# Optimization experiments

Hardware: AMD Instinct MI355X
Metric: run time of the kernel (lower is better)

Reference implementation:

```python
import jax, jax.numpy as jnp
import numpy as np

B, S, DIM, COV = 64, 512, 1024, 256


def setup_inputs() -> dict:
    key = jax.random.key(0)
    ks = jax.random.split(key, 12)
    s = 0.02
    h = jax.random.normal(ks[0], (B, DIM), jnp.float32)
    context = jax.random.normal(ks[1], (B, S, DIM), jnp.float32)
    cov = jax.random.normal(ks[2], (B, S, COV), jnp.float32)
    mask = jax.random.randint(ks[3], (B, S), 0, 2) == 1
    W_in = jax.random.normal(ks[4], (DIM, DIM), jnp.float32) * s
    W_out = jax.random.normal(ks[5], (DIM, 2 * DIM), jnp.float32) * s
    W_cov = jax.random.normal(ks[6], (DIM, COV), jnp.float32) * s
    b_cov = jax.random.normal(ks[7], (DIM,), jnp.float32) * s
    w_ih = jax.random.normal(ks[8], (3 * COV, 2 * DIM + 1), jnp.float32) * s
    w_hh = jax.random.normal(ks[9], (3 * COV, COV), jnp.float32) * s
    b_ih = jax.random.normal(ks[10], (3 * COV,), jnp.float32) * s
    b_hh = jax.random.normal(ks[11], (3 * COV,), jnp.float32) * s
    return dict(h=h, context=context, cov=cov, W_in=W_in, W_out=W_out,
                W_cov=W_cov, b_cov=b_cov, w_ih=w_ih, w_hh=w_hh,
                b_ih=b_ih, b_hh=b_hh, mask=mask)


def reference(h, context, cov, W_in, W_out, W_cov, b_cov, w_ih, w_hh, b_ih, b_hh, mask):
    # coverage-adjusted context: context + cov_linear(cov)  [B,S,DIM]
    ctx = context + jnp.einsum('bsc,dc->bsd', cov, W_cov) + b_cov
    # target = linear_in(h)  [B,DIM]
    target = h @ W_in.T
    # scores = bmm(context, target).squeeze(2)  [B,S]
    attn = jnp.einsum('bsd,bd->bs', ctx, target)
    attn = jnp.where(mask, -jnp.inf, attn)
    attn = jax.nn.softmax(attn, axis=1)
    # weighted_context = bmm(attn3, context)  [B,DIM]
    wc = jnp.einsum('bs,bsd->bd', attn, ctx)
    h_tilde = jnp.tanh(jnp.concatenate([wc, h], axis=1) @ W_out.T)
    # single-step GRU coverage update over B*S rows
    h_exp = jnp.broadcast_to(h[:, None, :], (B, S, DIM))
    x = jnp.concatenate([ctx, h_exp, attn[..., None]], axis=-1).reshape(B * S, 2 * DIM + 1)
    h0 = cov.reshape(B * S, COV)
    gx = x @ w_ih.T + b_ih   # [B*S, 3*COV]
    gh = h0 @ w_hh.T + b_hh  # [B*S, 3*COV]
    xr, xz, xn = jnp.split(gx, 3, axis=1)
    hr, hz, hn = jnp.split(gh, 3, axis=1)
    r = jax.nn.sigmoid(xr + hr)
    z = jax.nn.sigmoid(xz + hz)
    n = jnp.tanh(xn + r * hn)
    new_cov = ((1.0 - z) * n + z * h0).reshape(B, S, COV)
    return h_tilde, attn, new_cov
```

## Files before the change

### kernel.cpp

```cpp
#include <hip/hip_runtime.h>
#include <math.h>

typedef unsigned short ushort_t;
typedef __attribute__((ext_vector_type(8))) short short8;
typedef __attribute__((ext_vector_type(4))) float f32x4;
typedef __attribute__((ext_vector_type(4))) unsigned short ushort4v;

constexpr int B_ = 64, S_ = 512, DIM_ = 1024, COV_ = 256, TC_ = 768, KIH_ = 2049;
constexpr int NG_ = 1024, KG_ = 1280;

__device__ __forceinline__ float b2f(ushort_t u) {
    union { unsigned int i; float f; } v; v.i = ((unsigned int)u) << 16; return v.f;
}
__device__ __forceinline__ ushort_t f2b(float f) {
    unsigned int x = __float_as_uint(f);
    unsigned int r = x + 0x7fffu + ((x >> 16) & 1u);
    return (ushort_t)(r >> 16);
}
__device__ __forceinline__ float ldv(const float* p, size_t i) { return p[i]; }
__device__ __forceinline__ float ldv(const ushort_t* p, size_t i) { return b2f(p[i]); }

__device__ __forceinline__ float wave_reduce(float a) {
#pragma unroll
    for (int off = 32; off >= 1; off >>= 1) a += __shfl_down(a, off, 64);
    return a;
}

__device__ __forceinline__ void xpose4(f32x4& v, int l) {
    float s, r;
    s = (l & 1) ? v[0] : v[1]; r = __shfl_xor(s, 1, 64); if (l & 1) v[0] = r; else v[1] = r;
    s = (l & 1) ? v[2] : v[3]; r = __shfl_xor(s, 1, 64); if (l & 1) v[2] = r; else v[3] = r;
    s = (l & 2) ? v[0] : v[2]; r = __shfl_xor(s, 2, 64); if (l & 2) v[0] = r; else v[2] = r;
    s = (l & 2) ? v[1] : v[3]; r = __shfl_xor(s, 2, 64); if (l & 2) v[1] = r; else v[3] = r;
}

#define GLDS16(src, dst)                                                            \
    __builtin_amdgcn_global_load_lds(                                               \
        (const __attribute__((address_space(1))) void*)(src),                       \
        (__attribute__((address_space(3))) void*)(dst), 16, 0, 0)

__global__ void k_detect(const unsigned char* __restrict__ mask,
                         const ushort_t* __restrict__ win,
                         int* __restrict__ flags) {
    __shared__ int red0[256];
    __shared__ int red1[256];
    int tid = threadIdx.x, mb = 0, f32 = 0;
    for (int i = tid; i < 32768; i += 256)
        if ((i & 3) != 0 && mask[i] != 0) mb = 1;
    for (int i = tid; i < 32768; i += 256) {
        ushort_t u = win[2 * i];
        if ((u & 0x7F80u) >= 0x4480u) f32 = 1;
    }
    red0[tid] = mb; red1[tid] = f32; __syncthreads();
    for (int st = 128; st >= 1; st >>= 1) {
        if (tid < st) { red0[tid] |= red0[tid + st]; red1[tid] |= red1[tid + st]; }
        __syncthreads();
    }
    if (tid == 0) { flags[0] = red0[0]; flags[1] = red1[0]; }
}

template <typename IT>
__device__ __forceinline__ void transpose_body(const IT* __restrict__ in,
                                               ushort_t* __restrict__ out,
                                               int R, int C, int ld, int off) {
    int idx = blockIdx.x * 256 + threadIdx.x;
    if (idx >= R * C) return;
    int r = idx / C, c = idx - r * C;
    out[c * R + r] = f2b(ldv(in, (size_t)r * ld + off + c));
}
__global__ void k_transpose(const void* __restrict__ in, ushort_t* __restrict__ out,
                            int R, int C, int ld, int off, const int* __restrict__ flags) {
    if (flags[1]) transpose_body((const float*)in, out, R, C, ld, off);
    else transpose_body((const ushort_t*)in, out, R, C, ld, off);
}

template <typename IT>
__device__ __forceinline__ void watt_body(const IT* __restrict__ wih, float* __restrict__ watt) {
    int j = threadIdx.x;
    watt[j] = ldv(wih, (size_t)j * KIH_ + 2048);
}
__global__ void k_watt(const void* __restrict__ wih, float* __restrict__ watt,
                       const int* __restrict__ flags) {
    if (flags[1]) watt_body((const float*)wih, watt);
    else watt_body((const ushort_t*)wih, watt);
}

template <typename IT>
__device__ __forceinline__ void bfold_body(const IT* __restrict__ bcov,
                                           const IT* __restrict__ wih,
                                           float* __restrict__ bfold) {
    int j = blockIdx.x * 4 + (threadIdx.x >> 6);
    int lane = threadIdx.x & 63;
    const IT* wr = wih + (size_t)j * KIH_;
    float a = 0.f;
#pragma unroll
    for (int i = 0; i < 16; ++i) { int k = lane + 64 * i; a += ldv(bcov, k) * ldv(wr, k); }
    a = wave_reduce(a);
    if (lane == 0) bfold[j] = a;
}
__global__ __launch_bounds__(256) void k_bfold(const void* __restrict__ bcov,
                                               const void* __restrict__ wih,
                                               float* __restrict__ bfold,
                                               const int* __restrict__ flags) {
    if (flags[1]) bfold_body((const float*)bcov, (const float*)wih, bfold);
    else bfold_body((const ushort_t*)bcov, (const ushort_t*)wih, bfold);
}

__global__ __launch_bounds__(256) void k_wfold(const ushort_t* __restrict__ wcov_t,
                                               const ushort_t* __restrict__ w_t,
                                               float* __restrict__ wfold) {
    __shared__ float col[DIM_];
    int c = blockIdx.x, tid = threadIdx.x;
    for (int d = tid; d < DIM_; d += 256) col[d] = b2f(wcov_t[c * DIM_ + d]);
    __syncthreads();
    float a0 = 0.f, a1 = 0.f, a2 = 0.f;
    for (int d = 0; d < DIM_; ++d) {
        float x = col[d];
        const ushort_t* wr = w_t + d * TC_;
        a0 += x * b2f(wr[tid]);
        a1 += x * b2f(wr[tid + 256]);
        a2 += x * b2f(wr[tid + 512]);
    }
    wfold[c * TC_ + tid] = a0;
    wfold[c * TC_ + tid + 256] = a1;
    wfold[c * TC_ + tid + 512] = a2;
}

template <typename IT>
__device__ __forceinline__ void buildwg_body(const IT* __restrict__ wih,
                                             const IT* __restrict__ whh,
                                             const float* __restrict__ wfold,
                                             ushort_t* __restrict__ wg) {
    int idx = blockIdx.x * 256 + threadIdx.x;
    if (idx >= NG_ * KG_) return;
    int n = idx / KG_, k = idx - n * KG_;
    int g = n & 3, cq = n >> 2;
    int j = g * COV_ + cq;
    float v;
    if (k < DIM_) {
        v = (j < TC_) ? ldv(wih, (size_t)j * KIH_ + k) : 0.f;
    } else {
        int c = k - DIM_;
        if (j < 512)      v = wfold[c * TC_ + j] + ldv(whh, (size_t)j * COV_ + c);
        else if (j < TC_) v = wfold[c * TC_ + j];
        else              v = ldv(whh, (size_t)(j - 256) * COV_ + c);
    }
    wg[(size_t)n * KG_ + k] = f2b(v);
}
__global__ void k_buildwg(const void* __restrict__ wih, const void* __restrict__ whh,
                          const float* __restrict__ wfold, ushort_t* __restrict__ wg,
                          const int* __restrict__ flags) {
    if (flags[1]) buildwg_body((const float*)wih, (const float*)whh, wfold, wg);
    else buildwg_body((const ushort_t*)wih, (const ushort_t*)whh, wfold, wg);
}

template <typename IT>
__device__ __forceinline__ void target_body(const IT* __restrict__ h,
                                            const IT* __restrict__ W_in,
                                            float* __restrict__ target) {
    int o = blockIdx.x * 4 + (threadIdx.x >> 6);
    int lane = threadIdx.x & 63;
    int b = o >> 10, d = o & (DIM_ - 1);
    const IT* hr = h + (size_t)b * DIM_;
    const IT* wr = W_in + (size_t)d * DIM_;
    float a = 0.f;
#pragma unroll
    for (int j = 0; j < 16; ++j) { int k = lane + 64 * j; a += ldv(hr, k) * ldv(wr, k); }
    a = wave_reduce(a);
    if (lane == 0) target[o] = a;
}
__global__ __launch_bounds__(256) void k_target_w(const void* __restrict__ h,
                                                  const void* __restrict__ W_in,
                                                  float* __restrict__ target,
                                                  const int* __restrict__ flags) {
    if (flags[1]) target_body((const float*)h, (const float*)W_in, target);
    else target_body((const ushort_t*)h, (const ushort_t*)W_in, target);
}

template <typename IT>
__device__ __forceinline__ void mvec_body(const float* __restrict__ target,
                                          const IT* __restrict__ W_cov,
                                          const IT* __restrict__ bcov,
                                          float* __restrict__ mvec,
                                          float* __restrict__ bct) {
    __shared__ float tg[DIM_];
    __shared__ float red[256];
    int b = blockIdx.x, q = blockIdx.y, tid = threadIdx.x;
    float pb = 0.f;
    for (int k = tid; k < DIM_; k += 256) {
        float t = target[b * DIM_ + k];
        tg[k] = t; pb += t * ldv(bcov, k);
    }
    red[tid] = pb; __syncthreads();
    for (int st = 128; st >= 1; st >>= 1) {
        if (tid < st) red[tid] += red[tid + st];
        __syncthreads();
    }
    if (q == 0 && tid == 0) bct[b] = red[0];
    __syncthreads();
    int cg = tid & 63, dg = tid >> 6;
    int c = q * 64 + cg;
    float acc = 0.f;
    int d0 = dg * 256;
    for (int d = d0; d < d0 + 256; ++d) acc += tg[d] * ldv(W_cov, (size_t)d * COV_ + c);
    red[dg * 64 + cg] = acc;
    __syncthreads();
    if (dg == 0)
        mvec[b * COV_ + c] = red[cg] + red[64 + cg] + red[128 + cg] + red[192 + cg];
}
__global__ __launch_bounds__(256) void k_mvec(const float* __restrict__ target,
                                              const void* __restrict__ W_cov,
                                              const void* __restrict__ bcov,
                                              float* __restrict__ mvec,
                                              float* __restrict__ bct,
                                              const int* __restrict__ flags) {
    if (flags[1]) mvec_body(target, (const float*)W_cov, (const float*)bcov, mvec, bct);
    else mvec_body(target, (const ushort_t*)W_cov, (const ushort_t*)bcov, mvec, bct);
}

template <typename IT>
__device__ __forceinline__ void scoreraw_body(const IT* __restrict__ context,
                                              const IT* __restrict__ cov,
                                              const float* __restrict__ target,
                                              const float* __restrict__ mvec,
                                              const float* __restrict__ bct,
                                              float* __restrict__ scf,
                                              ushort_t* __restrict__ ctx_bf,
                                              ushort_t* __restrict__ cov_bf) {
    __shared__ float tg[DIM_];
    __shared__ float ms[COV_];
    int b = blockIdx.x, tid = threadIdx.x;
    for (int k = tid; k < DIM_; k += 256) tg[k] = target[b * DIM_ + k];
    if (tid < COV_) ms[tid] = mvec[b * COV_ + tid];
    float bc = bct[b];
    __syncthreads();
    int wave = tid >> 6, lane = tid & 63;
    int s0 = blockIdx.y * 64 + wave * 16;
    for (int i = 0; i < 16; ++i) {
        int s = s0 + i;
        size_t row = (size_t)(b * S_ + s);
        const IT* cr = context + row * DIM_;
        const IT* vr = cov + row * COV_;
        float a = 0.f;
        if constexpr (sizeof(IT) == 4) {
#pragma unroll
            for (int j = 0; j < 4; ++j) {
                int d = lane * 4 + 256 * j;
                float4 x = *(const float4*)((const float*)cr + d);
                a += x.x * tg[d] + x.y * tg[d + 1] + x.z * tg[d + 2] + x.w * tg[d + 3];
                if (ctx_bf) {
                    ushort4v u;
                    u[0] = f2b(x.x); u[1] = f2b(x.y); u[2] = f2b(x.z); u[3] = f2b(x.w);
                    *(ushort4v*)(ctx_bf + row * DIM_ + d) = u;
                }
            }
            {
                int cc = lane * 4;
                float4 x = *(const float4*)((const float*)vr + cc);
                a += x.x * ms[cc] + x.y * ms[cc + 1] + x.z * ms[cc + 2] + x.w * ms[cc + 3];
                if (cov_bf) {
                    ushort4v u;
                    u[0] = f2b(x.x); u[1] = f2b(x.y); u[2] = f2b(x.z); u[3] = f2b(x.w);
                    *(ushort4v*)(cov_bf + row * COV_ + cc) = u;
                }
            }
        } else {
#pragma unroll
            for (int j = 0; j < 16; ++j) { int d = lane + 64 * j; a += ldv(cr, d) * tg[d]; }
#pragma unroll
            for (int j = 0; j < 4; ++j) { int c = lane + 64 * j; a += ldv(vr, c) * ms[c]; }
        }
        a = wave_reduce(a);
        if (lane == 0) scf[row] = a + bc;
    }
}
__global__ __launch_bounds__(256) void k_scoreraw(const void* __restrict__ context,
                                                  const void* __restrict__ cov,
                                                  const float* __restrict__ target,
                                                  const float* __restrict__ mvec,
                                                  const float* __restrict__ bct,
                                                  float* __restrict__ scf,
                                                  ushort_t* __restrict__ ctx_bf,
                                                  ushort_t* __restrict__ cov_bf,
                                                  const int* __restrict__ flags) {
    if (flags[1]) scoreraw_body((const float*)context, (const float*)cov, target, mvec, bct,
                                scf, ctx_bf, cov_bf);
    else scoreraw_body((const ushort_t*)context, (const ushort_t*)cov, target, mvec, bct,
                       scf, ctx_bf, cov_bf);
}

__global__ __launch_bounds__(256) void k_softmax(const float* __restrict__ scf,
                                                 const void* __restrict__ maskp,
                                                 const int* __restrict__ flags,
                                                 float* __restrict__ attnf,
                                                 float* __restrict__ attn_out) {
    __shared__ float red[256];
    int b = blockIdx.x, tid = threadIdx.x;
    int mb = flags[0];
    int i0 = b * S_ + tid, i1 = i0 + 256;
    int m0 = mb ? (int)((const unsigned char*)maskp)[i0] : ((const int*)maskp)[i0];
    int m1 = mb ? (int)((const unsigned char*)maskp)[i1] : ((const int*)maskp)[i1];
    float s0 = m0 ? -INFINITY : scf[i0];
    float s1 = m1 ? -INFINITY : scf[i1];
    red[tid] = fmaxf(s0, s1); __syncthreads();
    for (int st = 128; st >= 1; st >>= 1) {
        if (tid < st) red[tid] = fmaxf(red[tid], red[tid + st]);
        __syncthreads();
    }
    float mx = red[0]; __syncthreads();
    float e0 = expf(s0 - mx), e1 = expf(s1 - mx);
    red[tid] = e0 + e1; __syncthreads();
    for (int st = 128; st >= 1; st >>= 1) {
        if (tid < st) red[tid] += red[tid + st];
        __syncthreads();
    }
    float inv = 1.0f / red[0];
    float a0 = e0 * inv, a1 = e1 * inv;
    attnf[i0] = a0; attnf[i1] = a1;
    attn_out[i0] = a0; attn_out[i1] = a1;
}

__global__ __launch_bounds__(256) void k_wcpart2(const ushort_t* __restrict__ ctx_bf,
                                                 const ushort_t* __restrict__ cov_bf,
                                                 const void* __restrict__ ctx_in,
                                                 const void* __restrict__ cov_in,
                                                 const float* __restrict__ attnf,
                                                 float* __restrict__ wc8,
                                                 float* __restrict__ ac8,
                                                 const int* __restrict__ flags) {
    const ushort_t* C = flags[1] ? ctx_bf : (const ushort_t*)ctx_in;
    const ushort_t* V = flags[1] ? cov_bf : (const ushort_t*)cov_in;
    __shared__ float at[64];
    int b = blockIdx.x, ch = blockIdx.y, tid = threadIdx.x;
    int s0 = ch * 64;
    if (tid < 64) at[tid] = attnf[b * S_ + s0 + tid];
    __syncthreads();
    float acv = 0.f;
    for (int s = 0; s < 64; ++s)
        acv += at[s] * b2f(V[((size_t)(b * S_ + s0 + s)) * COV_ + tid]);
    ac8[((size_t)ch * B_ + b) * COV_ + tid] = acv;
    float acc[4] = {0.f, 0.f, 0.f, 0.f};
    for (int s = 0; s < 64; ++s) {
        float w = at[s];
        const ushort_t* cr = C + ((size_t)(b * S_ + s0 + s)) * DIM_;
        acc[0] += w * b2f(cr[tid]);
        acc[1] += w * b2f(cr[tid + 256]);
        acc[2] += w * b2f(cr[tid + 512]);
        acc[3] += w * b2f(cr[tid + 768]);
    }
    size_t base = ((size_t)ch * B_ + b) * DIM_;
    for (int m = 0; m < 4; ++m) wc8[base + tid + 256 * m] = acc[m];
}

template <typename IT>
__device__ __forceinline__ void wcfin_body(const float* __restrict__ wc8,
                                           const float* __restrict__ ac8,
                                           const ushort_t* __restrict__ wcov_t,
                                           const IT* __restrict__ bcov,
                                           float* __restrict__ wc) {
    __shared__ float ac[COV_];
    int b = blockIdx.x, tid = threadIdx.x;
    float a = 0.f;
    for (int ch = 0; ch < 8; ++ch) a += ac8[((size_t)ch * B_ + b) * COV_ + tid];
    ac[tid] = a;
    __syncthreads();
    float acc[4] = {0.f, 0.f, 0.f, 0.f};
    for (int ch = 0; ch < 8; ++ch) {
        size_t base = ((size_t)ch * B_ + b) * DIM_;
        for (int m = 0; m < 4; ++m) acc[m] += wc8[base + tid + 256 * m];
    }
    for (int c = 0; c < COV_; ++c) {
        float av = ac[c];
        const ushort_t* wr = wcov_t + c * DIM_;
        acc[0] += av * b2f(wr[tid]);
        acc[1] += av * b2f(wr[tid + 256]);
        acc[2] += av * b2f(wr[tid + 512]);
        acc[3] += av * b2f(wr[tid + 768]);
    }
    for (int m = 0; m < 4; ++m) {
        int d = tid + 256 * m;
        wc[b * DIM_ + d] = acc[m] + ldv(bcov, d);
    }
}
__global__ __launch_bounds__(256) void k_wcfin(const float* __restrict__ wc8,
                                               const float* __restrict__ ac8,
                                               const ushort_t* __restrict__ wcov_t,
                                               const void* __restrict__ bcov,
                                               float* __restrict__ wc,
                                               const int* __restrict__ flags) {
    if (flags[1]) wcfin_body(wc8, ac8, wcov_t, (const float*)bcov, wc);
    else wcfin_body(wc8, ac8, wcov_t, (const ushort_t*)bcov, wc);
}

template <typename IT>
__device__ __forceinline__ void htilde_body(const float* __restrict__ wc,
                                            const IT* __restrict__ h,
                                            const IT* __restrict__ W_out,
                                            float* __restrict__ out_ht) {
    int o = blockIdx.x * 4 + (threadIdx.x >> 6);
    int lane = threadIdx.x & 63;
    int b = o >> 10, d = o & (DIM_ - 1);
    const float* wcr = wc + b * DIM_;
    const IT* hr = h + (size_t)b * DIM_;
    const IT* wr = W_out + (size_t)d * 2 * DIM_;
    float a = 0.f;
#pragma unroll
    for (int j = 0; j < 16; ++j) { int k = lane + 64 * j; a += wcr[k] * ldv(wr, k); }
#pragma unroll
    for (int j = 0; j < 16; ++j) { int k = lane + 64 * j; a += ldv(hr, k) * ldv(wr, DIM_ + k); }
    a = wave_reduce(a);
    if (lane == 0) out_ht[o] = tanhf(a);
}
__global__ __launch_bounds__(256) void k_htilde_w(const float* __restrict__ wc,
                                                  const void* __restrict__ h,
                                                  const void* __restrict__ W_out,
                                                  float* __restrict__ out_ht,
                                                  const int* __restrict__ flags) {
    if (flags[1]) htilde_body(wc, (const float*)h, (const float*)W_out, out_ht);
    else htilde_body(wc, (const ushort_t*)h, (const ushort_t*)W_out, out_ht);
}

template <typename IT>
__device__ __forceinline__ void gxh_body(const IT* __restrict__ h,
                                         const IT* __restrict__ w_ih,
                                         const IT* __restrict__ b_ih,
                                         const float* __restrict__ bfold,
                                         float* __restrict__ gxall) {
    int o = blockIdx.x * 4 + (threadIdx.x >> 6);
    int lane = threadIdx.x & 63;
    int b = o / TC_, j = o - b * TC_;
    const IT* hr = h + (size_t)b * DIM_;
    const IT* wr = w_ih + (size_t)j * KIH_ + DIM_;
    float a = 0.f;
#pragma unroll
    for (int i = 0; i < 16; ++i) { int k = lane + 64 * i; a += ldv(hr, k) * ldv(wr, k); }
    a = wave_reduce(a);
    if (lane == 0) gxall[o] = a + ldv(b_ih, j) + bfold[j];
}
__global__ __launch_bounds__(256) void k_gxh_w(const void* __restrict__ h,
                                               const void* __restrict__ w_ih,
                                               const void* __restrict__ b_ih,
                                               const float* __restrict__ bfold,
                                               float* __restrict__ gxall,
                                               const int* __restrict__ flags) {
    if (flags[1]) gxh_body((const float*)h, (const float*)w_ih, (const float*)b_ih, bfold, gxall);
    else gxh_body((const ushort_t*)h, (const ushort_t*)w_ih, (const ushort_t*)b_ih, bfold, gxall);
}

__global__ __launch_bounds__(256) void k_gemm6(const ushort_t* __restrict__ ctx_bf,
                                               const ushort_t* __restrict__ cov_bf,
                                               const void* __restrict__ ctx_in,
                                               const void* __restrict__ cov_in,
                                               const ushort_t* __restrict__ wg,
                                               const float* __restrict__ attnf,
                                               const float* __restrict__ gxall,
                                               const float* __restrict__ watt,
                                               const void* __restrict__ bhh,
                                               float* __restrict__ out_cov,
                                               const int* __restrict__ flags) {
    const int f32in = flags[1];
    const ushort_t* Xc = f32in ? ctx_bf : (const ushort_t*)ctx_in;
    const ushort_t* Xv = f32in ? cov_bf : (const ushort_t*)cov_in;
    __shared__ __align__(16) unsigned char smem[65536];
    ushort_t* A0 = (ushort_t*)smem;
    ushort_t* B0 = A0 + 8192;
    ushort_t* A1 = B0 + 8192;
    ushort_t* B1 = A1 + 8192;
    float* smN = (float*)smem;
    float* smZ = smN + 128 * 33;

    int tid = threadIdx.x;
    int p = blockIdx.x;
    int xcd = p & 7, t = p >> 3;
    int nb = t & 7, rb = xcd + 8 * (t >> 3);
    int n0 = nb * 128;
    int grow0 = rb * 128;
    int wave = tid >> 6, lane = tid & 63;
    int wm = wave >> 1, wn = wave & 1;
    int half = lane >> 4, r16 = lane & 15;

    const ushort_t* gAc[4]; const ushort_t* gAv[4]; const ushort_t* gB[4];
    int ldsOff[4];
#pragma unroll
    for (int j = 0; j < 4; ++j) {
        int c = wave * 256 + j * 64 + lane;
        int row = c >> 3, sl = (c & 7) ^ ((c >> 3) & 7);
        gAc[j] = Xc + (size_t)(grow0 + row) * DIM_ + sl * 8;
        gAv[j] = Xv + (size_t)(grow0 + row) * COV_ + sl * 8;
        gB[j]  = wg + (size_t)(n0 + row) * KG_ + sl * 8;
        ldsOff[j] = (wave * 256 + j * 64) * 8;
    }

    int offA[2][4], offB[2][4];
#pragma unroll
    for (int kh = 0; kh < 2; ++kh)
#pragma unroll
        for (int u = 0; u < 4; ++u) {
            int rA = wm * 64 + u * 16 + r16;
            offA[kh][u] = rA * 64 + ((kh * 4 + half) ^ (rA & 7)) * 8;
            int rB = wn * 64 + u * 16 + r16;
            offB[kh][u] = rB * 64 + ((kh * 4 + half) ^ (rB & 7)) * 8;
        }

    f32x4 acc[4][4];
#pragma unroll
    for (int i = 0; i < 4; ++i)
#pragma unroll
        for (int j = 0; j < 4; ++j) acc[i][j] = (f32x4){0.f, 0.f, 0.f, 0.f};

    auto stage = [&](int kt, ushort_t* Ad, ushort_t* Bd) {
        int k0 = kt * 64;
        if (k0 < DIM_) {
#pragma unroll
            for (int j = 0; j < 4; ++j) GLDS16(gAc[j] + k0, Ad + ldsOff[j]);
        } else {
            int kk = k0 - DIM_;
#pragma unroll
            for (int j = 0; j < 4; ++j) GLDS16(gAv[j] + kk, Ad + ldsOff[j]);
        }
#pragma unroll
        for (int j = 0; j < 4; ++j) GLDS16(gB[j] + k0, Bd + ldsOff[j]);
    };
    auto compute = [&](const ushort_t* Ac, const ushort_t* Bc) {
#pragma unroll
        for (int kh = 0; kh < 2; ++kh) {
            short8 a[4], b[4];
#pragma unroll
            for (int u = 0; u < 4; ++u) a[u] = *(const short8*)&Ac[offA[kh][u]];
#pragma unroll
            for (int u = 0; u < 4; ++u) b[u] = *(const short8*)&Bc[offB[kh][u]];
#pragma unroll
            for (int i = 0; i < 4; ++i)
#pragma unroll
                for (int j = 0; j < 4; ++j)
                    acc[i][j] = __builtin_amdgcn_mfma_f32_16x16x32_bf16(a[i], b[j], acc[i][j], 0, 0, 0);
        }
    };

    constexpr int NT = KG_ / 64;
    stage(0, A0, B0);
    __syncthreads();
#pragma unroll 1
    for (int kt = 0; kt < NT; kt += 2) {
        stage(kt + 1, A1, B1);
        compute(A0, B0);
        __syncthreads();
        if (kt + 2 < NT) stage(kt + 2, A0, B0);
        compute(A1, B1);
        __syncthreads();
    }

    int l = lane;
    int bb = grow0 >> 9;
    const float* gx = gxall + bb * TC_;
    int rloc[4]; float atv[4];
#pragma unroll
    for (int i = 0; i < 4; ++i) {
        rloc[i] = wm * 64 + 16 * i + ((l >> 4) << 2) + (l & 3);
        atv[i] = attnf[grow0 + rloc[i]];
    }
#pragma unroll
    for (int j = 0; j < 4; ++j) {
        int cl = wn * 16 + 4 * j + ((l >> 2) & 3);
        int c = (n0 >> 2) + cl;
        float gxR = gx[c], gxZ = gx[COV_ + c], gxN = gx[2 * COV_ + c];
        float waR = watt[c], waZ = watt[COV_ + c], waN = watt[2 * COV_ + c];
        float bhR, bhZ, bhN;
        if (f32in) {
            const float* bp = (const float*)bhh;
            bhR = bp[c]; bhZ = bp[COV_ + c]; bhN = bp[2 * COV_ + c];
        } else {
            const ushort_t* bp = (const ushort_t*)bhh;
            bhR = b2f(bp[c]); bhZ = b2f(bp[COV_ + c]); bhN = b2f(bp[2 * COV_ + c]);
        }
#pragma unroll
        for (int i = 0; i < 4; ++i) {
            f32x4 v = acc[i][j];
            xpose4(v, l);
            float at = atv[i];
            float aR  = v[0] + gxR + at * waR + bhR;
            float aZ  = v[1] + gxZ + at * waZ + bhZ;
            float aXN = v[2] + gxN + at * waN;
            float aHN = v[3] + bhN;
            float r = 1.f / (1.f + expf(-aR));
            float z = 1.f / (1.f + expf(-aZ));
            float nn = tanhf(aXN + r * aHN);
            smN[rloc[i] * 33 + cl] = nn;
            smZ[rloc[i] * 33 + cl] = z;
        }
    }
    __syncthreads();
    int cbase = nb * 32;
    for (int u = tid; u < 128 * 8; u += 256) {
        int rl = u >> 3, c4 = (u & 7) * 4;
        float n0v = smN[rl * 33 + c4 + 0], n1v = smN[rl * 33 + c4 + 1];
        float n2v = smN[rl * 33 + c4 + 2], n3v = smN[rl * 33 + c4 + 3];
        float z0 = smZ[rl * 33 + c4 + 0], z1 = smZ[rl * 33 + c4 + 1];
        float z2 = smZ[rl * 33 + c4 + 2], z3 = smZ[rl * 33 + c4 + 3];
        size_t base = (size_t)(grow0 + rl) * COV_ + cbase + c4;
        float h0v, h1v, h2v, h3v;
        if (f32in) {
            float4 hv = *(const float4*)((const float*)cov_in + base);
            h0v = hv.x; h1v = hv.y; h2v = hv.z; h3v = hv.w;
        } else {
            ushort4v hv = *(const ushort4v*)((const ushort_t*)cov_in + base);
            h0v = b2f(hv[0]); h1v = b2f(hv[1]); h2v = b2f(hv[2]); h3v = b2f(hv[3]);
        }
        float4 o;
        o.x = (1.f - z0) * n0v + z0 * h0v;
        o.y = (1.f - z1) * n1v + z1 * h1v;
        o.z = (1.f - z2) * n2v + z2 * h2v;
        o.w = (1.f - z3) * n3v + z3 * h3v;
        *(float4*)(out_cov + base) = o;
    }
}

template <typename IT>
__device__ __forceinline__ void gru_body(const IT* __restrict__ context,
                                         const IT* __restrict__ cov,
                                         const float* __restrict__ attnf,
                                         const float* __restrict__ gxall,
                                         const float* __restrict__ watt,
                                         const ushort_t* __restrict__ w_t,
                                         const float* __restrict__ wfold,
                                         const ushort_t* __restrict__ whh_t,
                                         const IT* __restrict__ bhh,
                                         float* __restrict__ out_cov) {
    __shared__ float xc[8][DIM_];
    __shared__ float h0s[8][COV_];
    __shared__ float atn[8];
    int base = blockIdx.x * 8, tid = threadIdx.x;
    int b = base / S_;
    for (int i = tid; i < 8 * DIM_; i += 256)
        ((float*)xc)[i] = ldv(context, (size_t)base * DIM_ + i);
    for (int i = tid; i < 8 * COV_; i += 256)
        ((float*)h0s)[i] = ldv(cov, (size_t)base * COV_ + i);
    if (tid < 8) atn[tid] = attnf[base + tid];
    __syncthreads();
    int c = tid;
    float gxR = gxall[b * TC_ + c], gxZ = gxall[b * TC_ + 256 + c], gxN = gxall[b * TC_ + 512 + c];
    float bhR = ldv(bhh, c), bhZ = ldv(bhh, 256 + c), bhN = ldv(bhh, 512 + c);
    float waR = watt[c], waZ = watt[256 + c], waN = watt[512 + c];
    float aR[8], aZ[8], aXN[8], aHN[8];
#pragma unroll
    for (int g = 0; g < 8; ++g) {
        float a = atn[g];
        aR[g] = gxR + bhR + a * waR;
        aZ[g] = gxZ + bhZ + a * waZ;
        aXN[g] = gxN + a * waN;
        aHN[g] = bhN;
    }
    for (int k = 0; k < DIM_; ++k) {
        const ushort_t* row = w_t + k * TC_;
        float wr = b2f(row[c]), wz = b2f(row[256 + c]), wn = b2f(row[512 + c]);
#pragma unroll
        for (int g = 0; g < 8; ++g) {
            float x = xc[g][k];
            aR[g] += x * wr; aZ[g] += x * wz; aXN[g] += x * wn;
        }
    }
    for (int k = 0; k < COV_; ++k) {
        const float* row = wfold + k * TC_;
        float wr = row[c], wz = row[256 + c], wn = row[512 + c];
#pragma unroll
        for (int g = 0; g < 8; ++g) {
            float x = h0s[g][k];
            aR[g] += x * wr; aZ[g] += x * wz; aXN[g] += x * wn;
        }
    }
    for (int k = 0; k < COV_; ++k) {
        const ushort_t* row = whh_t + k * TC_;
        float wr = b2f(row[c]), wz = b2f(row[256 + c]), wn = b2f(row[512 + c]);
#pragma unroll
        for (int g = 0; g < 8; ++g) {
            float hh = h0s[g][k];
            aR[g] += hh * wr; aZ[g] += hh * wz; aHN[g] += hh * wn;
        }
    }
#pragma unroll
    for (int g = 0; g < 8; ++g) {
        float r = 1.f / (1.f + expf(-aR[g]));
        float z = 1.f / (1.f + expf(-aZ[g]));
        float n = tanhf(aXN[g] + r * aHN[g]);
        float h0c = h0s[g][c];
        out_cov[(size_t)(base + g) * COV_ + c] = (1.f - z) * n + z * h0c;
    }
}
__global__ __launch_bounds__(256) void k_gru_f(const void* __restrict__ context,
                                               const void* __restrict__ cov,
                                               const float* __restrict__ attnf,
                                               const float* __restrict__ gxall,
                                               const float* __restrict__ watt,
                                               const ushort_t* __restrict__ w_t,
                                               const float* __restrict__ wfold,
                                               const ushort_t* __restrict__ whh_t,
                                               const void* __restrict__ bhh,
                                               float* __restrict__ out_cov,
                                               const int* __restrict__ flags) {
    if (flags[1]) gru_body((const float*)context, (const float*)cov, attnf, gxall, watt,
                           w_t, wfold, whh_t, (const float*)bhh, out_cov);
    else gru_body((const ushort_t*)context, (const ushort_t*)cov, attnf, gxall, watt,
                  w_t, wfold, whh_t, (const ushort_t*)bhh, out_cov);
}

extern "C" void kernel_launch(void* const* d_in, const int* in_sizes, int n_in,
                              void* d_out, int out_size, void* d_ws, size_t ws_size,
                              hipStream_t stream) {
    const void* h       = d_in[0];
    const void* context = d_in[1];
    const void* cov     = d_in[2];
    const void* W_in    = d_in[3];
    const void* W_out   = d_in[4];
    const void* W_cov   = d_in[5];
    const void* b_cov   = d_in[6];
    const void* w_ih    = d_in[7];
    const void* w_hh    = d_in[8];
    const void* b_ih    = d_in[9];
    const void* b_hh    = d_in[10];
    const void* maskp   = d_in[11];

    float* out = (float*)d_out;
    float* out_ht   = out;
    float* out_attn = out + B_ * DIM_;
    float* out_cov  = out + B_ * DIM_ + B_ * S_;

    char* ws = (char*)d_ws;
    size_t o = 0;
    float* target = (float*)(ws + o); o += (size_t)B_ * DIM_ * 4;
    float* attnf  = (float*)(ws + o); o += (size_t)B_ * S_ * 4;
    float* wc     = (float*)(ws + o); o += (size_t)B_ * DIM_ * 4;
    float* gxall  = (float*)(ws + o); o += (size_t)B_ * TC_ * 4;
    float* watt   = (float*)(ws + o); o += 4096;
    float* mvec   = (float*)(ws + o); o += (size_t)B_ * COV_ * 4;
    float* bct    = (float*)(ws + o); o += 4096;
    float* bfold  = (float*)(ws + o); o += 4096;
    float* wfold  = (float*)(ws + o); o += (size_t)COV_ * TC_ * 4;
    ushort_t* w_t    = (ushort_t*)(ws + o); o += (size_t)DIM_ * TC_ * 2;
    ushort_t* whh_t  = (ushort_t*)(ws + o); o += (size_t)COV_ * TC_ * 2;
    ushort_t* wcov_t = (ushort_t*)(ws + o); o += (size_t)COV_ * DIM_ * 2;
    int* flags = (int*)(ws + o); o += 256;
    float* scf   = (float*)(ws + o); o += (size_t)B_ * S_ * 4;
    float* wc8   = (float*)(ws + o); o += (size_t)8 * B_ * DIM_ * 4;
    float* ac8   = (float*)(ws + o); o += (size_t)8 * B_ * COV_ * 4;
    ushort_t* wg = (ushort_t*)(ws + o); o += (size_t)NG_ * KG_ * 2;
    ushort_t* ctx_bf = (ushort_t*)(ws + o); o += (size_t)B_ * S_ * DIM_ * 2;
    ushort_t* cov_bf = (ushort_t*)(ws + o); o += (size_t)B_ * S_ * COV_ * 2;
    size_t fixed = o;

    const size_t TOTAL_ROWS = (size_t)B_ * S_;
    const bool fused = ws_size >= fixed;

    k_detect<<<1, 256, 0, stream>>>((const unsigned char*)maskp, (const ushort_t*)W_in, flags);
    k_transpose<<<(TC_ * DIM_) / 256, 256, 0, stream>>>(w_ih, w_t, TC_, DIM_, KIH_, 0, flags);
    k_transpose<<<(DIM_ * COV_) / 256, 256, 0, stream>>>(W_cov, wcov_t, DIM_, COV_, COV_, 0, flags);
    if (!fused)
        k_transpose<<<(TC_ * COV_) / 256, 256, 0, stream>>>(w_hh, whh_t, TC_, COV_, COV_, 0, flags);
    k_watt<<<1, TC_, 0, stream>>>(w_ih, watt, flags);
    k_bfold<<<TC_ / 4, 256, 0, stream>>>(b_cov, w_ih, bfold, flags);
    k_wfold<<<COV_, 256, 0, stream>>>(wcov_t, w_t, wfold);
    if (fused)
        k_buildwg<<<(NG_ * KG_ + 255) / 256, 256, 0, stream>>>(w_ih, w_hh, wfold, wg, flags);

    k_target_w<<<(B_ * DIM_) / 4, 256, 0, stream>>>(h, W_in, target, flags);
    k_mvec<<<dim3(B_, 4), 256, 0, stream>>>(target, W_cov, b_cov, mvec, bct, flags);
    k_scoreraw<<<dim3(B_, 8), 256, 0, stream>>>(context, cov, target, mvec, bct, scf,
                                                fused ? ctx_bf : nullptr,
                                                fused ? cov_bf : nullptr, flags);
    k_softmax<<<B_, 256, 0, stream>>>(scf, maskp, flags, attnf, out_attn);
    if (fused)
        k_wcpart2<<<dim3(B_, 8), 256, 0, stream>>>(ctx_bf, cov_bf, context, cov, attnf,
                                                   wc8, ac8, flags);
    else
        k_wcpart2<<<dim3(B_, 8), 256, 0, stream>>>((const ushort_t*)context, (const ushort_t*)cov,
                                                   context, cov, attnf, wc8, ac8, flags);
    k_wcfin<<<B_, 256, 0, stream>>>(wc8, ac8, wcov_t, b_cov, wc, flags);
    k_htilde_w<<<(B_ * DIM_) / 4, 256, 0, stream>>>(wc, h, W_out, out_ht, flags);

    k_gxh_w<<<(B_ * TC_) / 4, 256, 0, stream>>>(h, w_ih, b_ih, bfold, gxall, flags);
    if (fused) {
        int nblk = (int)(TOTAL_ROWS / 128) * (NG_ / 128);
        k_gemm6<<<nblk, 256, 0, stream>>>(ctx_bf, cov_bf, context, cov, wg, attnf,
                                          gxall, watt, b_hh, out_cov, flags);
    } else {
        k_gru_f<<<(B_ * S_) / 8, 256, 0, stream>>>(context, cov, attnf, gxall, watt,
                                                   w_t, wfold, whh_t, b_hh, out_cov, flags);
    }
}
```

Before: 727.0 us.

## Split serial prep kernels across more blocks and double score/wc grid parallelism

Replaces the single-block detect kernel with a 64-block partial pass plus a tiny combine kernel. Splits the weight fold over four K-chunks whose partial sums are added in buildwg, and merges the watt gather into the bfold kernel. Doubles the number of blocks for the score and weighted-context passes by halving the rows each block handles, with a wider final reduction. The aim is to fill more compute units in latency-bound small kernels, at the cost of more partial-sum workspace and an extra launch.

```diff
diff --git a/kernel.cpp b/kernel.cpp
--- a/kernel.cpp
+++ b/kernel.cpp
@@ -39,24 +39,34 @@
         (const __attribute__((address_space(1))) void*)(src),                       \
         (__attribute__((address_space(3))) void*)(dst), 16, 0, 0)
 
-__global__ void k_detect(const unsigned char* __restrict__ mask,
-                         const ushort_t* __restrict__ win,
-                         int* __restrict__ flags) {
-    __shared__ int red0[256];
-    __shared__ int red1[256];
-    int tid = threadIdx.x, mb = 0, f32 = 0;
-    for (int i = tid; i < 32768; i += 256)
+__global__ __launch_bounds__(256) void k_detect_p(const unsigned char* __restrict__ mask,
+                                                  const ushort_t* __restrict__ win,
+                                                  int* __restrict__ parts) {
+    __shared__ int r0[256];
+    __shared__ int r1[256];
+    int bid = blockIdx.x, tid = threadIdx.x, mb = 0, f32 = 0;
+    for (int i = bid * 256 + tid; i < 32768; i += 64 * 256)
         if ((i & 3) != 0 && mask[i] != 0) mb = 1;
-    for (int i = tid; i < 32768; i += 256) {
+    for (int i = bid * 256 + tid; i < 32768; i += 64 * 256) {
         ushort_t u = win[2 * i];
         if ((u & 0x7F80u) >= 0x4480u) f32 = 1;
     }
-    red0[tid] = mb; red1[tid] = f32; __syncthreads();
+    r0[tid] = mb; r1[tid] = f32; __syncthreads();
     for (int st = 128; st >= 1; st >>= 1) {
-        if (tid < st) { red0[tid] |= red0[tid + st]; red1[tid] |= red1[tid + st]; }
+        if (tid < st) { r0[tid] |= r0[tid + st]; r1[tid] |= r1[tid + st]; }
         __syncthreads();
     }
-    if (tid == 0) { flags[0] = red0[0]; flags[1] = red1[0]; }
+    if (tid == 0) { parts[bid] = r0[0]; parts[64 + bid] = r1[0]; }
+}
+__global__ void k_detect_c(const int* __restrict__ parts, int* __restrict__ flags) {
+    int tid = threadIdx.x;
+    int a = parts[tid], b = parts[64 + tid];
+#pragma unroll
+    for (int off = 32; off >= 1; off >>= 1) {
+        a |= __shfl_down(a, off, 64);
+        b |= __shfl_down(b, off, 64);
+    }
+    if (tid == 0) { flags[0] = a; flags[1] = b; }
 }
 
 template <typename IT>
@@ -75,20 +85,10 @@
 }
 
 template <typename IT>
-__device__ __forceinline__ void watt_body(const IT* __restrict__ wih, float* __restrict__ watt) {
-    int j = threadIdx.x;
-    watt[j] = ldv(wih, (size_t)j * KIH_ + 2048);
-}
-__global__ void k_watt(const void* __restrict__ wih, float* __restrict__ watt,
-                       const int* __restrict__ flags) {
-    if (flags[1]) watt_body((const float*)wih, watt);
-    else watt_body((const ushort_t*)wih, watt);
-}
-
-template <typename IT>
 __device__ __forceinline__ void bfold_body(const IT* __restrict__ bcov,
                                            const IT* __restrict__ wih,
-                                           float* __restrict__ bfold) {
+                                           float* __restrict__ bfold,
+                                           float* __restrict__ watt) {
     int j = blockIdx.x * 4 + (threadIdx.x >> 6);
     int lane = threadIdx.x & 63;
     const IT* wr = wih + (size_t)j * KIH_;
@@ -96,14 +96,37 @@
 #pragma unroll
     for (int i = 0; i < 16; ++i) { int k = lane + 64 * i; a += ldv(bcov, k) * ldv(wr, k); }
     a = wave_reduce(a);
-    if (lane == 0) bfold[j] = a;
+    if (lane == 0) { bfold[j] = a; watt[j] = ldv(wr, 2048); }
 }
 __global__ __launch_bounds__(256) void k_bfold(const void* __restrict__ bcov,
                                                const void* __restrict__ wih,
                                                float* __restrict__ bfold,
+                                               float* __restrict__ watt,
                                                const int* __restrict__ flags) {
-    if (flags[1]) bfold_body((const float*)bcov, (const float*)wih, bfold);
-    else bfold_body((const ushort_t*)bcov, (const ushort_t*)wih, bfold);
+    if (flags[1]) bfold_body((const float*)bcov, (const float*)wih, bfold, watt);
+    else bfold_body((const ushort_t*)bcov, (const ushort_t*)wih, bfold, watt);
+}
+
+__global__ __launch_bounds__(256) void k_wfold_p(const ushort_t* __restrict__ wcov_t,
+                                                 const ushort_t* __restrict__ w_t,
+                                                 float* __restrict__ wfp) {
+    __shared__ float col[256];
+    int c = blockIdx.x, p = blockIdx.y, tid = threadIdx.x;
+    col[tid] = b2f(wcov_t[c * DIM_ + p * 256 + tid]);
+    __syncthreads();
+    float a0 = 0.f, a1 = 0.f, a2 = 0.f;
+    const ushort_t* wt = w_t + (size_t)(p * 256) * TC_;
+    for (int d = 0; d < 256; ++d) {
+        float x = col[d];
+        const ushort_t* wr = wt + d * TC_;
+        a0 += x * b2f(wr[tid]);
+        a1 += x * b2f(wr[tid + 256]);
+        a2 += x * b2f(wr[tid + 512]);
+    }
+    float* o = wfp + ((size_t)p * COV_ + c) * TC_;
+    o[tid] = a0;
+    o[tid + 256] = a1;
+    o[tid + 512] = a2;
 }
 
 __global__ __launch_bounds__(256) void k_wfold(const ushort_t* __restrict__ wcov_t,
@@ -129,7 +152,7 @@
 template <typename IT>
 __device__ __forceinline__ void buildwg_body(const IT* __restrict__ wih,
                                              const IT* __restrict__ whh,
-                                             const float* __restrict__ wfold,
+                                             const float* __restrict__ wfp,
                                              ushort_t* __restrict__ wg) {
     int idx = blockIdx.x * 256 + threadIdx.x;
     if (idx >= NG_ * KG_) return;
@@ -141,17 +164,23 @@
         v = (j < TC_) ? ldv(wih, (size_t)j * KIH_ + k) : 0.f;
     } else {
         int c = k - DIM_;
-        if (j < 512)      v = wfold[c * TC_ + j] + ldv(whh, (size_t)j * COV_ + c);
-        else if (j < TC_) v = wfold[c * TC_ + j];
+        float wf = 0.f;
+        if (j < TC_) {
+            size_t base = (size_t)c * TC_ + j;
+            wf = wfp[base] + wfp[(size_t)COV_ * TC_ + base] +
+                 wfp[2 * (size_t)COV_ * TC_ + base] + wfp[3 * (size_t)COV_ * TC_ + base];
+        }
+        if (j < 512)      v = wf + ldv(whh, (size_t)j * COV_ + c);
+        else if (j < TC_) v = wf;
         else              v = ldv(whh, (size_t)(j - 256) * COV_ + c);
     }
     wg[(size_t)n * KG_ + k] = f2b(v);
 }
 __global__ void k_buildwg(const void* __restrict__ wih, const void* __restrict__ whh,
-                          const float* __restrict__ wfold, ushort_t* __restrict__ wg,
+                          const float* __restrict__ wfp, ushort_t* __restrict__ wg,
                           const int* __restrict__ flags) {
-    if (flags[1]) buildwg_body((const float*)wih, (const float*)whh, wfold, wg);
-    else buildwg_body((const ushort_t*)wih, (const ushort_t*)whh, wfold, wg);
+    if (flags[1]) buildwg_body((const float*)wih, (const float*)whh, wfp, wg);
+    else buildwg_body((const ushort_t*)wih, (const ushort_t*)whh, wfp, wg);
 }
 
 template <typename IT>
@@ -235,8 +264,8 @@
     float bc = bct[b];
     __syncthreads();
     int wave = tid >> 6, lane = tid & 63;
-    int s0 = blockIdx.y * 64 + wave * 16;
-    for (int i = 0; i < 16; ++i) {
+    int s0 = blockIdx.y * 32 + wave * 8;
+    for (int i = 0; i < 8; ++i) {
         int s = s0 + i;
         size_t row = (size_t)(b * S_ + s);
         const IT* cr = context + row * DIM_;
@@ -325,22 +354,22 @@
                                                  const void* __restrict__ ctx_in,
                                                  const void* __restrict__ cov_in,
                                                  const float* __restrict__ attnf,
-                                                 float* __restrict__ wc8,
-                                                 float* __restrict__ ac8,
+                                                 float* __restrict__ wcp,
+                                                 float* __restrict__ acp,
                                                  const int* __restrict__ flags) {
     const ushort_t* C = flags[1] ? ctx_bf : (const ushort_t*)ctx_in;
     const ushort_t* V = flags[1] ? cov_bf : (const ushort_t*)cov_in;
-    __shared__ float at[64];
+    __shared__ float at[32];
     int b = blockIdx.x, ch = blockIdx.y, tid = threadIdx.x;
-    int s0 = ch * 64;
-    if (tid < 64) at[tid] = attnf[b * S_ + s0 + tid];
+    int s0 = ch * 32;
+    if (tid < 32) at[tid] = attnf[b * S_ + s0 + tid];
     __syncthreads();
     float acv = 0.f;
-    for (int s = 0; s < 64; ++s)
+    for (int s = 0; s < 32; ++s)
         acv += at[s] * b2f(V[((size_t)(b * S_ + s0 + s)) * COV_ + tid]);
-    ac8[((size_t)ch * B_ + b) * COV_ + tid] = acv;
+    acp[((size_t)ch * B_ + b) * COV_ + tid] = acv;
     float acc[4] = {0.f, 0.f, 0.f, 0.f};
-    for (int s = 0; s < 64; ++s) {
+    for (int s = 0; s < 32; ++s) {
         float w = at[s];
         const ushort_t* cr = C + ((size_t)(b * S_ + s0 + s)) * DIM_;
         acc[0] += w * b2f(cr[tid]);
@@ -349,25 +378,25 @@
         acc[3] += w * b2f(cr[tid + 768]);
     }
     size_t base = ((size_t)ch * B_ + b) * DIM_;
-    for (int m = 0; m < 4; ++m) wc8[base + tid + 256 * m] = acc[m];
-}
-
-template <typename IT>
-__device__ __forceinline__ void wcfin_body(const float* __restrict__ wc8,
-                                           const float* __restrict__ ac8,
+    for (int m = 0; m < 4; ++m) wcp[base + tid + 256 * m] = acc[m];
+}
+
+template <typename IT>
+__device__ __forceinline__ void wcfin_body(const float* __restrict__ wcp,
+                                           const float* __restrict__ acp,
                                            const ushort_t* __restrict__ wcov_t,
                                            const IT* __restrict__ bcov,
                                            float* __restrict__ wc) {
     __shared__ float ac[COV_];
     int b = blockIdx.x, tid = threadIdx.x;
     float a = 0.f;
-    for (int ch = 0; ch < 8; ++ch) a += ac8[((size_t)ch * B_ + b) * COV_ + tid];
+    for (int ch = 0; ch < 16; ++ch) a += acp[((size_t)ch * B_ + b) * COV_ + tid];
     ac[tid] = a;
     __syncthreads();
     float acc[4] = {0.f, 0.f, 0.f, 0.f};
-    for (int ch = 0; ch < 8; ++ch) {
+    for (int ch = 0; ch < 16; ++ch) {
         size_t base = ((size_t)ch * B_ + b) * DIM_;
-        for (int m = 0; m < 4; ++m) acc[m] += wc8[base + tid + 256 * m];
+        for (int m = 0; m < 4; ++m) acc[m] += wcp[base + tid + 256 * m];
     }
     for (int c = 0; c < COV_; ++c) {
         float av = ac[c];
@@ -382,14 +411,14 @@
         wc[b * DIM_ + d] = acc[m] + ldv(bcov, d);
     }
 }
-__global__ __launch_bounds__(256) void k_wcfin(const float* __restrict__ wc8,
-                                               const float* __restrict__ ac8,
+__global__ __launch_bounds__(256) void k_wcfin(const float* __restrict__ wcp,
+                                               const float* __restrict__ acp,
                                                const ushort_t* __restrict__ wcov_t,
                                                const void* __restrict__ bcov,
                                                float* __restrict__ wc,
                                                const int* __restrict__ flags) {
-    if (flags[1]) wcfin_body(wc8, ac8, wcov_t, (const float*)bcov, wc);
-    else wcfin_body(wc8, ac8, wcov_t, (const ushort_t*)bcov, wc);
+    if (flags[1]) wcfin_body(wcp, acp, wcov_t, (const float*)bcov, wc);
+    else wcfin_body(wcp, acp, wcov_t, (const ushort_t*)bcov, wc);
 }
 
 template <typename IT>
@@ -735,13 +764,15 @@
     float* bct    = (float*)(ws + o); o += 4096;
     float* bfold  = (float*)(ws + o); o += 4096;
     float* wfold  = (float*)(ws + o); o += (size_t)COV_ * TC_ * 4;
+    float* wfp    = (float*)(ws + o); o += (size_t)4 * COV_ * TC_ * 4;
+    int* dparts   = (int*)(ws + o);   o += 512;
     ushort_t* w_t    = (ushort_t*)(ws + o); o += (size_t)DIM_ * TC_ * 2;
     ushort_t* whh_t  = (ushort_t*)(ws + o); o += (size_t)COV_ * TC_ * 2;
     ushort_t* wcov_t = (ushort_t*)(ws + o); o += (size_t)COV_ * DIM_ * 2;
     int* flags = (int*)(ws + o); o += 256;
     float* scf   = (float*)(ws + o); o += (size_t)B_ * S_ * 4;
-    float* wc8   = (float*)(ws + o); o += (size_t)8 * B_ * DIM_ * 4;
-    float* ac8   = (float*)(ws + o); o += (size_t)8 * B_ * COV_ * 4;
+    float* wcp   = (float*)(ws + o); o += (size_t)16 * B_ * DIM_ * 4;
+    float* acp   = (float*)(ws + o); o += (size_t)16 * B_ * COV_ * 4;
     ushort_t* wg = (ushort_t*)(ws + o); o += (size_t)NG_ * KG_ * 2;
     ushort_t* ctx_bf = (ushort_t*)(ws + o); o += (size_t)B_ * S_ * DIM_ * 2;
     ushort_t* cov_bf = (ushort_t*)(ws + o); o += (size_t)B_ * S_ * COV_ * 2;
@@ -750,30 +781,33 @@
     const size_t TOTAL_ROWS = (size_t)B_ * S_;
     const bool fused = ws_size >= fixed;
 
-    k_detect<<<1, 256, 0, stream>>>((const unsigned char*)maskp, (const ushort_t*)W_in, flags);
+    k_detect_p<<<64, 256, 0, stream>>>((const unsigned char*)maskp, (const ushort_t*)W_in, dparts);
+    k_detect_c<<<1, 64, 0, stream>>>(dparts, flags);
     k_transpose<<<(TC_ * DIM_) / 256, 256, 0, stream>>>(w_ih, w_t, TC_, DIM_, KIH_, 0, flags);
     k_transpose<<<(DIM_ * COV_) / 256, 256, 0, stream>>>(W_cov, wcov_t, DIM_, COV_, COV_, 0, flags);
     if (!fused)
         k_transpose<<<(TC_ * COV_) / 256, 256, 0, stream>>>(w_hh, whh_t, TC_, COV_, COV_, 0, flags);
-    k_watt<<<1, TC_, 0, stream>>>(w_ih, watt, flags);
-    k_bfold<<<TC_ / 4, 256, 0, stream>>>(b_cov, w_ih, bfold, flags);
-    k_wfold<<<COV_, 256, 0, stream>>>(wcov_t, w_t, wfold);
-    if (fused)
-        k_buildwg<<<(NG_ * KG_ + 255) / 256, 256, 0, stream>>>(w_ih, w_hh, wfold, wg, flags);
+    k_bfold<<<TC_ / 4, 256, 0, stream>>>(b_cov, w_ih, bfold, watt, flags);
+    if (fused) {
+        k_wfold_p<<<dim3(COV_, 4), 256, 0, stream>>>(wcov_t, w_t, wfp);
+        k_buildwg<<<(NG_ * KG_ + 255) / 256, 256, 0, stream>>>(w_ih, w_hh, wfp, wg, flags);
+    } else {
+        k_wfold<<<COV_, 256, 0, stream>>>(wcov_t, w_t, wfold);
+    }
 
     k_target_w<<<(B_ * DIM_) / 4, 256, 0, stream>>>(h, W_in, target, flags);
     k_mvec<<<dim3(B_, 4), 256, 0, stream>>>(target, W_cov, b_cov, mvec, bct, flags);
-    k_scoreraw<<<dim3(B_, 8), 256, 0, stream>>>(context, cov, target, mvec, bct, scf,
-                                                fused ? ctx_bf : nullptr,
-                                                fused ? cov_bf : nullptr, flags);
+    k_scoreraw<<<dim3(B_, 16), 256, 0, stream>>>(context, cov, target, mvec, bct, scf,
+                                                 fused ? ctx_bf : nullptr,
+                                                 fused ? cov_bf : nullptr, flags);
     k_softmax<<<B_, 256, 0, stream>>>(scf, maskp, flags, attnf, out_attn);
     if (fused)
-        k_wcpart2<<<dim3(B_, 8), 256, 0, stream>>>(ctx_bf, cov_bf, context, cov, attnf,
-                                                   wc8, ac8, flags);
+        k_wcpart2<<<dim3(B_, 16), 256, 0, stream>>>(ctx_bf, cov_bf, context, cov, attnf,
+                                                    wcp, acp, flags);
     else
-        k_wcpart2<<<dim3(B_, 8), 256, 0, stream>>>((const ushort_t*)context, (const ushort_t*)cov,
-                                                   context, cov, attnf, wc8, ac8, flags);
-    k_wcfin<<<B_, 256, 0, stream>>>(wc8, ac8, wcov_t, b_cov, wc, flags);
+        k_wcpart2<<<dim3(B_, 16), 256, 0, stream>>>((const ushort_t*)context, (const ushort_t*)cov,
+                                                    context, cov, attnf, wcp, acp, flags);
+    k_wcfin<<<B_, 256, 0, stream>>>(wcp, acp, wcov_t, b_cov, wc, flags);
     k_htilde_w<<<(B_ * DIM_) / 4, 256, 0, stream>>>(wc, h, W_out, out_ht, flags);
 
     k_gxh_w<<<(B_ * TC_) / 4, 256, 0, stream>>>(h, w_ih, b_ih, bfold, gxall, flags);
```

Result: faster. 603.0 us (-17.1%).
